# Optimization experiments

Measured on AMD Instinct MI355X. Metric: run time of the kernel, lower is better.

The kernel has to match this reference:

```python
import jax, jax.numpy as jnp
import numpy as np
import math

B, L, DIM = 128, 192, 512
NTOKEN = 100
MAX_BONDS = 6
MAX_LEN = 192


def _sinusoidal_pe(max_len, dim):
    pos = np.arange(max_len, dtype=np.float32)[:, None]
    div = np.exp(np.arange(0, dim, 2, dtype=np.float32) * (-math.log(10000.0) / dim))
    pe = np.zeros((max_len, dim), dtype=np.float32)
    pe[:, 0::2] = np.sin(pos * div)
    pe[:, 1::2] = np.cos(pos * div)
    return jnp.asarray(pe[:, None, :])  # [max_len, 1, dim]


def setup_inputs() -> dict:
    key = jax.random.key(0)
    ks = jax.random.split(key, 16)
    s = 0.02
    inp = {
        "element": jax.random.randint(ks[0], (B, L), 0, NTOKEN),
        "bond": jax.random.randint(ks[1], (B, L, MAX_BONDS), 0, L),
        "aroma": jax.random.randint(ks[2], (B, L), 0, 2),
        "charge": jax.random.randint(ks[3], (B, L), 0, 6),
        "segment": jax.random.randint(ks[4], (B, L), 0, 30),
        # parameters
        "pe": _sinusoidal_pe(MAX_LEN, DIM),
        "E_elem": jax.random.normal(ks[5], (NTOKEN, DIM), jnp.float32) * s,
        "E_charge": jax.random.normal(ks[6], (13, DIM), jnp.float32) * s,
        "E_aroma": jax.random.normal(ks[7], (2, DIM), jnp.float32) * s,
        "E_seg": jax.random.normal(ks[8], (30, DIM), jnp.float32) * s,
        "W1": jax.random.normal(ks[9], (DIM, 4 * DIM), jnp.float32) * s,
        "b1": jnp.zeros((4 * DIM,), jnp.float32),
        "W2": jax.random.normal(ks[10], (4 * DIM, DIM), jnp.float32) * s,
        "b2": jnp.zeros((DIM,), jnp.float32),
        "W3": jax.random.normal(ks[11], (DIM, 4 * DIM), jnp.float32) * s,
        "b3": jnp.zeros((4 * DIM,), jnp.float32),
        "W4": jax.random.normal(ks[12], (4 * DIM, DIM), jnp.float32) * s,
        "b4": jnp.zeros((DIM,), jnp.float32),
        "W5": jax.random.normal(ks[13], (DIM, DIM), jnp.float32) * s,
        "b5": jnp.zeros((DIM,), jnp.float32),
    }
    return inp


def _mlp(x, W1, b1, W2, b2, W3, b3, W4, b4, W5, b5):
    x = x + jnp.maximum(x @ W1 + b1, 0.0) @ W2 + b2
    x = x + jnp.maximum(x @ W3 + b3, 0.0) @ W4 + b4
    return x @ W5 + b5


def reference(element, bond, aroma, charge, segment, pe,
              E_elem, E_charge, E_aroma, E_seg,
              W1, b1, W2, b2, W3, b3, W4, b4, W5, b5):
    b, l = element.shape
    # embeddings: all [l, b, dim]
    emb = E_elem[element.T]
    emb = emb + pe[:l]                      # [l,1,dim] broadcast (eval: dropout off)
    emb = emb + E_aroma[aroma.T]
    emb = emb + E_charge[charge.T + 6]
    emb = emb + E_seg[segment.T]
    message = _mlp(emb, W1, b1, W2, b2, W3, b3, W4, b4, W5, b5)  # [l,b,dim]
    # bond aggregation: agg[k] = sum_m message[bond[b,k,m]] excluding self-bonds
    # (equivalent to the dense one-hot einsum with the diagonal masked out)
    msg_bld = jnp.transpose(message, (1, 0, 2))          # [b,l,dim]
    g = msg_bld[jnp.arange(b)[:, None, None], bond]      # [b,l,MAX_BONDS,dim]
    mask = (bond != jnp.arange(l)[None, :, None]).astype(message.dtype)
    agg = jnp.einsum('bkmd,bkm->bkd', g, mask)           # [b,l,dim]
    return emb + jnp.transpose(agg, (1, 0, 2))           # [l,b,dim]
```

## Files before the change

kernel.cpp:

```cpp
#include <hip/hip_runtime.h>
#include <cstdint>
#include <cstddef>

typedef unsigned short u16;
typedef unsigned int u32;

typedef unsigned short u16x8 __attribute__((ext_vector_type(8)));
typedef __bf16 bf16x8 __attribute__((ext_vector_type(8)));
typedef float f32x4 __attribute__((ext_vector_type(4)));
typedef float f32x8 __attribute__((ext_vector_type(8)));

#define NB   128
#define NL   192
#define NTOK (NB * NL)
#define DIM  512
#define HID  2048

static __device__ __forceinline__ float bf2f(u16 h) {
    union { u32 u; float f; } v; v.u = ((u32)h) << 16; return v.f;
}
static __device__ __forceinline__ u16 f2bf(float f) {
    union { float f; u32 u; } v; v.f = f;
    u32 u = v.u + 0x7FFF + ((v.u >> 16) & 1);
    return (u16)(u >> 16);
}

__global__ void transpose_all(const float* __restrict__ W1, u16* __restrict__ W1T,
                              const float* __restrict__ W2, u16* __restrict__ W2T,
                              const float* __restrict__ W3, u16* __restrict__ W3T,
                              const float* __restrict__ W4, u16* __restrict__ W4T,
                              const float* __restrict__ W5, u16* __restrict__ W5T) {
    int bid = blockIdx.x;
    const float* in; u16* out; int K, N, t;
    if (bid < 1024)      { in = W1; out = W1T; K = DIM; N = HID; t = bid; }
    else if (bid < 2048) { in = W2; out = W2T; K = HID; N = DIM; t = bid - 1024; }
    else if (bid < 3072) { in = W3; out = W3T; K = DIM; N = HID; t = bid - 2048; }
    else if (bid < 4096) { in = W4; out = W4T; K = HID; N = DIM; t = bid - 3072; }
    else                 { in = W5; out = W5T; K = DIM; N = DIM; t = bid - 4096; }
    const int nx = N >> 5;
    const int n0 = (t % nx) * 32, k0 = (t / nx) * 32;
    __shared__ float tile[32][33];
    int tx = threadIdx.x & 31, ty = threadIdx.x >> 5;
#pragma unroll
    for (int i = 0; i < 4; i++)
        tile[ty + i * 8][tx] = in[(size_t)(k0 + ty + i * 8) * N + n0 + tx];
    __syncthreads();
#pragma unroll
    for (int i = 0; i < 4; i++)
        out[(size_t)(n0 + ty + i * 8) * K + k0 + tx] = f2bf(tile[tx][ty + i * 8]);
}

static __device__ __forceinline__ void add8f(float* acc, const float* p) {
    f32x8 v = *(const f32x8*)p;
#pragma unroll
    for (int i = 0; i < 8; i++) acc[i] += v[i];
}

__global__ void embed_kernel(const int* __restrict__ element, const int* __restrict__ aroma,
                             const int* __restrict__ charge, const int* __restrict__ segment,
                             const float* __restrict__ pe, const float* __restrict__ E_elem,
                             const float* __restrict__ E_charge, const float* __restrict__ E_aroma,
                             const float* __restrict__ E_seg,
                             float* __restrict__ emb32, u16* __restrict__ emb16) {
    int t = blockIdx.x * 4 + (threadIdx.x >> 6);
    int lane = threadIdx.x & 63;
    int l = t >> 7, b = t & 127;
    int d = lane * 8;
    int idx = b * NL + l;
    int e = element[idx];
    int a = aroma[idx];
    int c = charge[idx] + 6;
    int s = segment[idx];
    float acc[8] = {0, 0, 0, 0, 0, 0, 0, 0};
    add8f(acc, E_elem  + (size_t)e * DIM + d);
    add8f(acc, pe      + (size_t)l * DIM + d);
    add8f(acc, E_aroma + (size_t)a * DIM + d);
    add8f(acc, E_charge+ (size_t)c * DIM + d);
    add8f(acc, E_seg   + (size_t)s * DIM + d);
    f32x8 o32; u16x8 o16;
#pragma unroll
    for (int i = 0; i < 8; i++) { o32[i] = acc[i]; o16[i] = f2bf(acc[i]); }
    *(f32x8*)(emb32 + (size_t)t * DIM + d) = o32;
    *(u16x8*)(emb16 + (size_t)t * DIM + d) = o16;
}

__global__ __launch_bounds__(512, 2) void gemm_bt(
    const u16* __restrict__ A, const u16* __restrict__ BT,
    const float* __restrict__ bias, const u16* __restrict__ resid16,
    const float* __restrict__ resid32,
    u16* __restrict__ C, int M, int N, int K, int do_relu) {
    __shared__ __align__(16) u16 smem[256 * 264];

    const int tid  = threadIdx.x;
    const int wave = tid >> 6;
    const int lane = tid & 63;

    const int nwg = gridDim.x;
    const int bid = blockIdx.x;
    const int wg  = ((nwg & 7) == 0) ? ((bid & 7) * (nwg >> 3) + (bid >> 3)) : bid;
    const int nt  = N >> 8;
    const int m0  = (wg / nt) * 256;
    const int n0  = (wg % nt) * 256;

    const int wmh = wave >> 2;
    const int wnq = wave & 3;
    const int fr  = lane & 15;
    const int fq  = lane >> 4;
    const int ck0 = ((fq ^ (fr & 7)) * 8);
    const int ck1 = (((4 | fq) ^ (fr & 7)) * 8);

    const int sRow = tid >> 3;
    const int sChk = ((tid & 7) ^ (sRow & 7)) * 8;
    const int ldst = sRow * 64 + (tid & 7) * 8;

    const u16* Asrc = A  + (size_t)(m0 + sRow) * K + sChk;
    const u16* Bsrc = BT + (size_t)(n0 + sRow) * K + sChk;

    f32x4 acc[8][4] = {};

#define GLL(gp, lp) __builtin_amdgcn_global_load_lds(                            \
        (const __attribute__((address_space(1))) void*)(gp),                     \
        (__attribute__((address_space(3))) void*)(lp), 16, 0, 0)
#define STAGE(buf, kt) do {                                                      \
    GLL(Asrc + (size_t)(kt) * 64,                 &smem[(buf)*16384 +        ldst]); \
    GLL(Bsrc + (size_t)(kt) * 64,                 &smem[32768 + (buf)*16384 +        ldst]); \
    GLL(Asrc + (size_t)(kt) * 64 + (size_t) 64*K, &smem[(buf)*16384 +  4096 + ldst]); \
    GLL(Bsrc + (size_t)(kt) * 64 + (size_t) 64*K, &smem[32768 + (buf)*16384 +  4096 + ldst]); \
    GLL(Asrc + (size_t)(kt) * 64 + (size_t)128*K, &smem[(buf)*16384 +  8192 + ldst]); \
    GLL(Bsrc + (size_t)(kt) * 64 + (size_t)128*K, &smem[32768 + (buf)*16384 +  8192 + ldst]); \
    GLL(Asrc + (size_t)(kt) * 64 + (size_t)192*K, &smem[(buf)*16384 + 12288 + ldst]); \
    GLL(Bsrc + (size_t)(kt) * 64 + (size_t)192*K, &smem[32768 + (buf)*16384 + 12288 + ldst]); \
} while (0)

    const int nk = K >> 6;
    STAGE(0, 0);

    for (int t = 0; t < nk; ++t) {
        asm volatile("s_waitcnt vmcnt(0)\n\ts_barrier" ::: "memory");
        if (t + 1 < nk) STAGE((t + 1) & 1, t + 1);

        const u16* Ab = &smem[(t & 1) * 16384];
        const u16* Bb = &smem[32768 + (t & 1) * 16384];
#pragma unroll
        for (int s = 0; s < 2; ++s) {
            const int ck = s ? ck1 : ck0;
            bf16x8 af[8], bg[4];
#pragma unroll
            for (int i = 0; i < 8; ++i)
                af[i] = *(const bf16x8*)(&Ab[(wmh * 128 + i * 16 + fr) * 64 + ck]);
#pragma unroll
            for (int j = 0; j < 4; ++j)
                bg[j] = *(const bf16x8*)(&Bb[(wnq * 64 + j * 16 + fr) * 64 + ck]);

            __builtin_amdgcn_s_setprio(1);
#pragma unroll
            for (int i = 0; i < 8; ++i)
#pragma unroll
                for (int j = 0; j < 4; ++j)
                    acc[i][j] = __builtin_amdgcn_mfma_f32_16x16x32_bf16(
                        af[i], bg[j], acc[i][j], 0, 0, 0);
            __builtin_amdgcn_s_setprio(0);
        }
    }
#undef STAGE
#undef GLL

    __syncthreads();
#define CSTR 264
#pragma unroll
    for (int j = 0; j < 4; j++) {
        int n = n0 + wnq * 64 + j * 16 + fr;
        float bv = bias[n];
#pragma unroll
        for (int i = 0; i < 8; i++) {
#pragma unroll
            for (int r = 0; r < 4; r++) {
                int m = m0 + wmh * 128 + i * 16 + fq * 4 + r;
                float v = acc[i][j][r] + bv;
                if (do_relu) v = fmaxf(v, 0.0f);
                if (resid16) v += bf2f(resid16[(size_t)m * N + n]);
                if (resid32) v += resid32[(size_t)m * N + n];
                smem[(wmh * 128 + i * 16 + fq * 4 + r) * CSTR + wnq * 64 + j * 16 + fr] = f2bf(v);
            }
        }
    }
    __syncthreads();
    {
        const int erow = tid >> 5;
        const int ecol = (tid & 31) * 8;
#pragma unroll
        for (int rr = 0; rr < 16; ++rr) {
            int row = rr * 16 + erow;
            *(u16x8*)(C + (size_t)(m0 + row) * N + n0 + ecol) =
                *(const u16x8*)(&smem[row * CSTR + ecol]);
        }
    }
#undef CSTR
}

__global__ void agg_kernel(const float* __restrict__ emb32, const u16* __restrict__ msg,
                           const int* __restrict__ bond, float* __restrict__ out) {
    int t = blockIdx.x * 4 + (threadIdx.x >> 6);
    int lane = threadIdx.x & 63;
    int l = t >> 7, b = t & 127;
    int d = lane * 8;
    float acc[8];
    {
        f32x8 v = *(const f32x8*)(emb32 + (size_t)t * DIM + d);
#pragma unroll
        for (int i = 0; i < 8; i++) acc[i] = v[i];
    }
    const int* bp = bond + ((size_t)b * NL + l) * 6;
#pragma unroll
    for (int m = 0; m < 6; m++) {
        int j = bp[m];
        if (j != l) {
            u16x8 g = *(const u16x8*)(msg + ((size_t)j * NB + b) * DIM + d);
#pragma unroll
            for (int i = 0; i < 8; i++) acc[i] += bf2f(g[i]);
        }
    }
    f32x8 o;
#pragma unroll
    for (int i = 0; i < 8; i++) o[i] = acc[i];
    *(f32x8*)(out + (size_t)t * DIM + d) = o;
}

extern "C" void kernel_launch(void* const* d_in, const int* in_sizes, int n_in,
                              void* d_out, int out_size, void* d_ws, size_t ws_size,
                              hipStream_t stream) {
    const int* element = (const int*)d_in[0];
    const int* bond    = (const int*)d_in[1];
    const int* aroma   = (const int*)d_in[2];
    const int* charge  = (const int*)d_in[3];
    const int* segment = (const int*)d_in[4];
    const float* pe      = (const float*)d_in[5];
    const float* E_elem  = (const float*)d_in[6];
    const float* E_charge= (const float*)d_in[7];
    const float* E_aroma = (const float*)d_in[8];
    const float* E_seg   = (const float*)d_in[9];
    const float* W1 = (const float*)d_in[10];
    const float* b1 = (const float*)d_in[11];
    const float* W2 = (const float*)d_in[12];
    const float* b2 = (const float*)d_in[13];
    const float* W3 = (const float*)d_in[14];
    const float* b3 = (const float*)d_in[15];
    const float* W4 = (const float*)d_in[16];
    const float* b4 = (const float*)d_in[17];
    const float* W5 = (const float*)d_in[18];
    const float* b5 = (const float*)d_in[19];

    float* emb32 = (float*)d_out;

    char* ws = (char*)d_ws;
    size_t woff = 0;
    auto take = [&](size_t bytes) -> u16* {
        u16* p = (u16*)(ws + woff);
        woff += (bytes + 255) & ~(size_t)255;
        return p;
    };
    u16* W1T = take((size_t)HID * DIM * 2);
    u16* W2T = take((size_t)DIM * HID * 2);
    u16* W3T = take((size_t)HID * DIM * 2);
    u16* W4T = take((size_t)DIM * HID * 2);
    u16* W5T = take((size_t)DIM * DIM * 2);
    u16* emb16 = take((size_t)NTOK * DIM * 2);
    u16* msg   = take((size_t)NTOK * DIM * 2);

    static const int ncs[] = {1, 2, 3, 4, 6, 8, 12, 16, 24, 32, 48, 96};
    int CM = 256;
    for (int nc : ncs) {
        int cm = NTOK / nc;
        if (cm % 256 != 0) continue;
        size_t need = woff + ((size_t)cm * HID * 2 + 256)
                           + ((size_t)cm * DIM * 2 + 256) * 2;
        if (need <= ws_size) { CM = cm; break; }
    }
    u16* hC  = take((size_t)CM * HID * 2);
    u16* xaC = take((size_t)CM * DIM * 2);
    u16* xbC = take((size_t)CM * DIM * 2);

    transpose_all<<<4352, 256, 0, stream>>>(W1, W1T, W2, W2T, W3, W3T,
                                            W4, W4T, W5, W5T);

    embed_kernel<<<NTOK / 4, 256, 0, stream>>>(element, aroma, charge, segment, pe,
                                               E_elem, E_charge, E_aroma, E_seg,
                                               emb32, emb16);

    for (int c0 = 0; c0 < NTOK; c0 += CM) {
        const u16* x16 = emb16 + (size_t)c0 * DIM;
        const float* x32 = emb32 + (size_t)c0 * DIM;
        u16* msgC = msg + (size_t)c0 * DIM;
        int mt = CM / 256;
        gemm_bt<<<dim3(mt * (HID / 256)), 512, 0, stream>>>(x16, W1T, b1, nullptr, nullptr, hC,  CM, HID, DIM, 1);
        gemm_bt<<<dim3(mt * (DIM / 256)), 512, 0, stream>>>(hC,  W2T, b2, nullptr, x32,     xaC, CM, DIM, HID, 0);
        gemm_bt<<<dim3(mt * (HID / 256)), 512, 0, stream>>>(xaC, W3T, b3, nullptr, nullptr, hC,  CM, HID, DIM, 1);
        gemm_bt<<<dim3(mt * (DIM / 256)), 512, 0, stream>>>(hC,  W4T, b4, xaC,    nullptr,  xbC, CM, DIM, HID, 0);
        gemm_bt<<<dim3(mt * (DIM / 256)), 512, 0, stream>>>(xbC, W5T, b5, nullptr, nullptr, msgC, CM, DIM, DIM, 0);
    }

    agg_kernel<<<NTOK / 4, 256, 0, stream>>>(emb32, msg, bond, (float*)d_out);
}
```

Baseline: 480.8 us.

## Triple-buffer A tiles in GEMM and drop fp32 embedding copy

The GEMM now stages A tiles two k-steps ahead in a three-slot LDS ring, while B stays double-buffered, and waits with a partial vmcnt so outstanding loads can overlap compute. The embedding kernel writes only a bf16 copy. The W2 residual and the final aggregation read that bf16 copy instead of an fp32 buffer, which cuts memory traffic. This trades output precision on the embedding term and raises LDS use to 160KB, which may lower occupancy below two blocks per CU.

```diff
diff --git a/kernel.cpp b/kernel.cpp
--- a/kernel.cpp
+++ b/kernel.cpp
@@ -61,7 +61,7 @@
                              const float* __restrict__ pe, const float* __restrict__ E_elem,
                              const float* __restrict__ E_charge, const float* __restrict__ E_aroma,
                              const float* __restrict__ E_seg,
-                             float* __restrict__ emb32, u16* __restrict__ emb16) {
+                             u16* __restrict__ emb16) {
     int t = blockIdx.x * 4 + (threadIdx.x >> 6);
     int lane = threadIdx.x & 63;
     int l = t >> 7, b = t & 127;
@@ -77,19 +77,17 @@
     add8f(acc, E_aroma + (size_t)a * DIM + d);
     add8f(acc, E_charge+ (size_t)c * DIM + d);
     add8f(acc, E_seg   + (size_t)s * DIM + d);
-    f32x8 o32; u16x8 o16;
-#pragma unroll
-    for (int i = 0; i < 8; i++) { o32[i] = acc[i]; o16[i] = f2bf(acc[i]); }
-    *(f32x8*)(emb32 + (size_t)t * DIM + d) = o32;
+    u16x8 o16;
+#pragma unroll
+    for (int i = 0; i < 8; i++) o16[i] = f2bf(acc[i]);
     *(u16x8*)(emb16 + (size_t)t * DIM + d) = o16;
 }
 
 __global__ __launch_bounds__(512, 2) void gemm_bt(
     const u16* __restrict__ A, const u16* __restrict__ BT,
     const float* __restrict__ bias, const u16* __restrict__ resid16,
-    const float* __restrict__ resid32,
     u16* __restrict__ C, int M, int N, int K, int do_relu) {
-    __shared__ __align__(16) u16 smem[256 * 264];
+    __shared__ __align__(16) u16 smem[81920];
 
     const int tid  = threadIdx.x;
     const int wave = tid >> 6;
@@ -121,26 +119,36 @@
 #define GLL(gp, lp) __builtin_amdgcn_global_load_lds(                            \
         (const __attribute__((address_space(1))) void*)(gp),                     \
         (__attribute__((address_space(3))) void*)(lp), 16, 0, 0)
-#define STAGE(buf, kt) do {                                                      \
-    GLL(Asrc + (size_t)(kt) * 64,                 &smem[(buf)*16384 +        ldst]); \
-    GLL(Bsrc + (size_t)(kt) * 64,                 &smem[32768 + (buf)*16384 +        ldst]); \
+#define STAGE_A(buf, kt) do {                                                    \
+    GLL(Asrc + (size_t)(kt) * 64,                 &smem[(buf)*16384 +         ldst]); \
     GLL(Asrc + (size_t)(kt) * 64 + (size_t) 64*K, &smem[(buf)*16384 +  4096 + ldst]); \
-    GLL(Bsrc + (size_t)(kt) * 64 + (size_t) 64*K, &smem[32768 + (buf)*16384 +  4096 + ldst]); \
     GLL(Asrc + (size_t)(kt) * 64 + (size_t)128*K, &smem[(buf)*16384 +  8192 + ldst]); \
-    GLL(Bsrc + (size_t)(kt) * 64 + (size_t)128*K, &smem[32768 + (buf)*16384 +  8192 + ldst]); \
     GLL(Asrc + (size_t)(kt) * 64 + (size_t)192*K, &smem[(buf)*16384 + 12288 + ldst]); \
-    GLL(Bsrc + (size_t)(kt) * 64 + (size_t)192*K, &smem[32768 + (buf)*16384 + 12288 + ldst]); \
 } while (0)
+#define STAGE_B(buf, kt) do {                                                    \
+    GLL(Bsrc + (size_t)(kt) * 64,                 &smem[49152 + (buf)*16384 +         ldst]); \
+    GLL(Bsrc + (size_t)(kt) * 64 + (size_t) 64*K, &smem[49152 + (buf)*16384 +  4096 + ldst]); \
+    GLL(Bsrc + (size_t)(kt) * 64 + (size_t)128*K, &smem[49152 + (buf)*16384 +  8192 + ldst]); \
+    GLL(Bsrc + (size_t)(kt) * 64 + (size_t)192*K, &smem[49152 + (buf)*16384 + 12288 + ldst]); \
+} while (0)
 
     const int nk = K >> 6;
-    STAGE(0, 0);
-
+    STAGE_A(0, 0); STAGE_B(0, 0); STAGE_A(1, 1);
+
+    int bt3 = 0;
     for (int t = 0; t < nk; ++t) {
-        asm volatile("s_waitcnt vmcnt(0)\n\ts_barrier" ::: "memory");
-        if (t + 1 < nk) STAGE((t + 1) & 1, t + 1);
-
-        const u16* Ab = &smem[(t & 1) * 16384];
-        const u16* Bb = &smem[32768 + (t & 1) * 16384];
+        if (t < nk - 1)
+            asm volatile("s_waitcnt vmcnt(4)\n\ts_barrier" ::: "memory");
+        else
+            asm volatile("s_waitcnt vmcnt(0)\n\ts_barrier" ::: "memory");
+        if (t + 1 < nk) STAGE_B((t + 1) & 1, t + 1);
+        if (t + 2 < nk) {
+            int a3 = bt3 + 2; if (a3 >= 3) a3 -= 3;
+            STAGE_A(a3, t + 2);
+        }
+
+        const u16* Ab = &smem[bt3 * 16384];
+        const u16* Bb = &smem[49152 + (t & 1) * 16384];
 #pragma unroll
         for (int s = 0; s < 2; ++s) {
             const int ck = s ? ck1 : ck0;
@@ -161,8 +169,10 @@
                         af[i], bg[j], acc[i][j], 0, 0, 0);
             __builtin_amdgcn_s_setprio(0);
         }
-    }
-#undef STAGE
+        bt3 = (bt3 == 2) ? 0 : bt3 + 1;
+    }
+#undef STAGE_A
+#undef STAGE_B
 #undef GLL
 
     __syncthreads();
@@ -179,7 +189,6 @@
                 float v = acc[i][j][r] + bv;
                 if (do_relu) v = fmaxf(v, 0.0f);
                 if (resid16) v += bf2f(resid16[(size_t)m * N + n]);
-                if (resid32) v += resid32[(size_t)m * N + n];
                 smem[(wmh * 128 + i * 16 + fq * 4 + r) * CSTR + wnq * 64 + j * 16 + fr] = f2bf(v);
             }
         }
@@ -198,7 +207,7 @@
 #undef CSTR
 }
 
-__global__ void agg_kernel(const float* __restrict__ emb32, const u16* __restrict__ msg,
+__global__ void agg_kernel(const u16* __restrict__ emb16, const u16* __restrict__ msg,
                            const int* __restrict__ bond, float* __restrict__ out) {
     int t = blockIdx.x * 4 + (threadIdx.x >> 6);
     int lane = threadIdx.x & 63;
@@ -206,9 +215,9 @@
     int d = lane * 8;
     float acc[8];
     {
-        f32x8 v = *(const f32x8*)(emb32 + (size_t)t * DIM + d);
-#pragma unroll
-        for (int i = 0; i < 8; i++) acc[i] = v[i];
+        u16x8 v = *(const u16x8*)(emb16 + (size_t)t * DIM + d);
+#pragma unroll
+        for (int i = 0; i < 8; i++) acc[i] = bf2f(v[i]);
     }
     const int* bp = bond + ((size_t)b * NL + l) * 6;
 #pragma unroll
@@ -250,8 +259,6 @@
     const float* W5 = (const float*)d_in[18];
     const float* b5 = (const float*)d_in[19];
 
-    float* emb32 = (float*)d_out;
-
     char* ws = (char*)d_ws;
     size_t woff = 0;
     auto take = [&](size_t bytes) -> u16* {
@@ -285,19 +292,18 @@
 
     embed_kernel<<<NTOK / 4, 256, 0, stream>>>(element, aroma, charge, segment, pe,
                                                E_elem, E_charge, E_aroma, E_seg,
-                                               emb32, emb16);
+                                               emb16);
 
     for (int c0 = 0; c0 < NTOK; c0 += CM) {
         const u16* x16 = emb16 + (size_t)c0 * DIM;
-        const float* x32 = emb32 + (size_t)c0 * DIM;
         u16* msgC = msg + (size_t)c0 * DIM;
         int mt = CM / 256;
-        gemm_bt<<<dim3(mt * (HID / 256)), 512, 0, stream>>>(x16, W1T, b1, nullptr, nullptr, hC,  CM, HID, DIM, 1);
-        gemm_bt<<<dim3(mt * (DIM / 256)), 512, 0, stream>>>(hC,  W2T, b2, nullptr, x32,     xaC, CM, DIM, HID, 0);
-        gemm_bt<<<dim3(mt * (HID / 256)), 512, 0, stream>>>(xaC, W3T, b3, nullptr, nullptr, hC,  CM, HID, DIM, 1);
-        gemm_bt<<<dim3(mt * (DIM / 256)), 512, 0, stream>>>(hC,  W4T, b4, xaC,    nullptr,  xbC, CM, DIM, HID, 0);
-        gemm_bt<<<dim3(mt * (DIM / 256)), 512, 0, stream>>>(xbC, W5T, b5, nullptr, nullptr, msgC, CM, DIM, DIM, 0);
-    }
-
-    agg_kernel<<<NTOK / 4, 256, 0, stream>>>(emb32, msg, bond, (float*)d_out);
-}
+        gemm_bt<<<dim3(mt * (HID / 256)), 512, 0, stream>>>(x16, W1T, b1, nullptr, hC,  CM, HID, DIM, 1);
+        gemm_bt<<<dim3(mt * (DIM / 256)), 512, 0, stream>>>(hC,  W2T, b2, x16,    xaC, CM, DIM, HID, 0);
+        gemm_bt<<<dim3(mt * (HID / 256)), 512, 0, stream>>>(xaC, W3T, b3, nullptr, hC,  CM, HID, DIM, 1);
+        gemm_bt<<<dim3(mt * (DIM / 256)), 512, 0, stream>>>(hC,  W4T, b4, xaC,    xbC, CM, DIM, HID, 0);
+        gemm_bt<<<dim3(mt * (DIM / 256)), 512, 0, stream>>>(xbC, W5T, b5, nullptr, msgC, CM, DIM, DIM, 0);
+    }
+
+    agg_kernel<<<NTOK / 4, 256, 0, stream>>>(emb16, msg, bond, (float*)d_out);
+}
```

Measured after the change: 453.2 us. -5.7%, faster.
